# Kernel tuning notes

Hardware: AMD Instinct MI355X
Metric: run time of the kernel (lower is better)

The kernel has to match this reference:

```python
import jax, jax.numpy as jnp
import numpy as np

GAE_GAMMA = 0.99
GAE_LAMBDA = 0.95
T, N_ENVS = 4096, 2048


def setup_inputs() -> dict:
    key = jax.random.key(0)
    k1, k2, k3, k4 = jax.random.split(key, 4)
    rewards = jax.random.normal(k1, (T, N_ENVS), dtype=jnp.float32)
    values = jax.random.normal(k2, (T, N_ENVS), dtype=jnp.float32)
    next_values = jax.random.normal(k3, (T, N_ENVS), dtype=jnp.float32)
    next_dones = jax.random.randint(k4, (T, N_ENVS), 0, 2).astype(jnp.bool_)
    return {"rewards": rewards, "values": values,
            "next_values": next_values, "next_dones": next_dones}


def reference(rewards, values, next_values, next_dones):
    gamma = jnp.asarray(GAE_GAMMA, rewards.dtype)
    lam = jnp.asarray(GAE_LAMBDA, rewards.dtype)
    not_done = 1.0 - next_dones.astype(rewards.dtype)  # ~next_dones
    # deltas[t] = r[t] + gamma * V(s_{t+1}) * ~done[t] - V(s_t)
    deltas = rewards + gamma * next_values * not_done - values
    gae_discount = gamma * lam

    def step(running_gae, inp):
        delta_t, nd_t = inp
        g = delta_t + gae_discount * nd_t * running_gae
        return g, g

    init = jnp.zeros_like(rewards[0])
    # reverse-time scan over the recurrence
    _, adv = jax.lax.scan(step, init, (deltas, not_done), reverse=True)
    returns = adv + values
    return adv, returns
```

## Files before the change

kernel.cpp:

```cpp
#include <hip/hip_runtime.h>

#define TT    4096
#define NENV  2048
#define N4    (NENV / 4)
#define L     8
#define NCH   (TT / L)
#define NCGRP 2
#define NBLK  (NCH * NCGRP)
#define SUP   8
#define NSUP  (NCH / SUP)

#define GAMMA 0.99f
#define GL    (0.99f * 0.95f)

#define STEP_AB(r_, v_, nv_, dn_, A_, B_)                    \
    {                                                        \
        const float nd = (dn_) ? 0.0f : 1.0f;                \
        const float di = (r_) + GAMMA * (nv_) * nd - (v_);   \
        const float c  = GL * nd;                            \
        (B_) = di + c * (B_);                                \
        (A_) = c * (A_);                                     \
    }

#define STEP_OUT(r_, v_, nv_, dn_, g_, adv_, ret_)           \
    {                                                        \
        const float nd = (dn_) ? 0.0f : 1.0f;                \
        const float di = (r_) + GAMMA * (nv_) * nd - (v_);   \
        (g_) = di + GL * nd * (g_);                          \
        (adv_) = (g_);                                       \
        (ret_) = (g_) + (v_);                                \
    }

#define COMPOSE(Aj_, Bj_, A_, B_)                            \
    {                                                        \
        (B_) = (Bj_) + (Aj_) * (B_);                         \
        (A_) = (Aj_) * (A_);                                 \
    }

__global__ __launch_bounds__(256) void gae_k1(
    const float4* __restrict__ r4,  const float4* __restrict__ v4,
    const float4* __restrict__ nv4, const int4*   __restrict__ dn4,
    float4* __restrict__ wsA, float4* __restrict__ wsB)
{
    const int chunk = blockIdx.x / NCGRP;
    const int c4    = (blockIdx.x % NCGRP) * 256 + threadIdx.x;
    const int t0    = chunk * L;

    float Ax = 1.0f, Ay = 1.0f, Az = 1.0f, Aw = 1.0f;
    float Bx = 0.0f, By = 0.0f, Bz = 0.0f, Bw = 0.0f;
#pragma unroll
    for (int i = L - 1; i >= 0; --i) {
        const int idx = (t0 + i) * N4 + c4;
        const float4 r  = r4[idx];
        const float4 v  = v4[idx];
        const float4 nv = nv4[idx];
        const int4   dn = dn4[idx];
        STEP_AB(r.x, v.x, nv.x, dn.x, Ax, Bx);
        STEP_AB(r.y, v.y, nv.y, dn.y, Ay, By);
        STEP_AB(r.z, v.z, nv.z, dn.z, Az, Bz);
        STEP_AB(r.w, v.w, nv.w, dn.w, Aw, Bw);
    }
    wsA[chunk * N4 + c4] = make_float4(Ax, Ay, Az, Aw);
    wsB[chunk * N4 + c4] = make_float4(Bx, By, Bz, Bw);
}

__global__ __launch_bounds__(256) void gae_k2a(
    const float4* __restrict__ wsA, const float4* __restrict__ wsB,
    float4* __restrict__ supA, float4* __restrict__ supB)
{
    const int t  = blockIdx.x * 256 + threadIdx.x;
    const int s  = t >> 9;
    const int c4 = t & (N4 - 1);

    float Ax = 1.0f, Ay = 1.0f, Az = 1.0f, Aw = 1.0f;
    float Bx = 0.0f, By = 0.0f, Bz = 0.0f, Bw = 0.0f;
#pragma unroll
    for (int j = s * SUP + SUP - 1; j >= s * SUP; --j) {
        const float4 Aj = wsA[j * N4 + c4];
        const float4 Bj = wsB[j * N4 + c4];
        COMPOSE(Aj.x, Bj.x, Ax, Bx);
        COMPOSE(Aj.y, Bj.y, Ay, By);
        COMPOSE(Aj.z, Bj.z, Az, Bz);
        COMPOSE(Aj.w, Bj.w, Aw, Bw);
    }
    supA[s * N4 + c4] = make_float4(Ax, Ay, Az, Aw);
    supB[s * N4 + c4] = make_float4(Bx, By, Bz, Bw);
}

__global__ __launch_bounds__(64) void gae_k2b(
    const float* __restrict__ supA, const float* __restrict__ supB,
    float* __restrict__ gSup)
{
    const int col = blockIdx.x * 64 + threadIdx.x;
    float g = 0.0f;
#pragma unroll 8
    for (int s = NSUP - 1; s >= 0; --s) {
        gSup[s * NENV + col] = g;
        g = supB[s * NENV + col] + supA[s * NENV + col] * g;
    }
}

__global__ __launch_bounds__(256) void gae_k3(
    const float4* __restrict__ r4,  const float4* __restrict__ v4,
    const float4* __restrict__ nv4, const int4*   __restrict__ dn4,
    const float4* __restrict__ wsA, const float4* __restrict__ wsB,
    const float4* __restrict__ gSup4,
    float4* __restrict__ adv4, float4* __restrict__ ret4)
{
    const int chunk = blockIdx.x / NCGRP;
    const int c4    = (blockIdx.x % NCGRP) * 256 + threadIdx.x;
    const int s     = chunk / SUP;
    const int t0    = chunk * L;

    const float4 g0 = gSup4[s * N4 + c4];
    float gx = g0.x, gy = g0.y, gz = g0.z, gw = g0.w;
    for (int j = s * SUP + SUP - 1; j > chunk; --j) {
        const float4 Aj = wsA[j * N4 + c4];
        const float4 Bj = wsB[j * N4 + c4];
        gx = Bj.x + Aj.x * gx;
        gy = Bj.y + Aj.y * gy;
        gz = Bj.z + Aj.z * gz;
        gw = Bj.w + Aj.w * gw;
    }

#pragma unroll
    for (int i = L - 1; i >= 0; --i) {
        const int idx = (t0 + i) * N4 + c4;
        const float4 r  = r4[idx];
        const float4 v  = v4[idx];
        const float4 nv = nv4[idx];
        const int4   dn = dn4[idx];
        float4 a, t;
        STEP_OUT(r.x, v.x, nv.x, dn.x, gx, a.x, t.x);
        STEP_OUT(r.y, v.y, nv.y, dn.y, gy, a.y, t.y);
        STEP_OUT(r.z, v.z, nv.z, dn.z, gz, a.z, t.z);
        STEP_OUT(r.w, v.w, nv.w, dn.w, gw, a.w, t.w);
        adv4[idx] = a;
        ret4[idx] = t;
    }
}

extern "C" void kernel_launch(void* const* d_in, const int* in_sizes, int n_in,
                              void* d_out, int out_size, void* d_ws, size_t ws_size,
                              hipStream_t stream) {
    const float4* r4  = (const float4*)d_in[0];
    const float4* v4  = (const float4*)d_in[1];
    const float4* nv4 = (const float4*)d_in[2];
    const int4*   dn4 = (const int4*)d_in[3];

    float4* adv4 = (float4*)d_out;
    float4* ret4 = adv4 + (size_t)TT * N4;

    float4* wsA  = (float4*)d_ws;
    float4* wsB  = wsA  + (size_t)NCH * N4;
    float4* supA = wsB  + (size_t)NCH * N4;
    float4* supB = supA + (size_t)NSUP * N4;
    float4* gSup = supB + (size_t)NSUP * N4;

    gae_k1<<<NBLK, 256, 0, stream>>>(r4, v4, nv4, dn4, wsA, wsB);
    gae_k2a<<<(NSUP * N4) / 256, 256, 0, stream>>>(wsA, wsB, supA, supB);
    gae_k2b<<<NENV / 64, 64, 0, stream>>>((const float*)supA, (const float*)supB,
                                          (float*)gSup);
    gae_k3<<<NBLK, 256, 0, stream>>>(r4, v4, nv4, dn4, wsA, wsB,
                                     (const float4*)gSup, adv4, ret4);
}
```

Before: 202.9 us.

## Replace two-level chunk scan with single sequential carry scan and batched loads

The hierarchical middle stage (super-chunk compose plus serial scan plus per-chunk recomposition in the final kernel) is replaced by one kernel that serially walks all 512 chunk carries per column. It uses double-buffered register prefetch of 16 chunks and writes the incoming carry for each chunk in place over the B workspace. The first and last kernels now issue all eight timesteps' loads up front into registers, with an occupancy hint, to raise memory-level parallelism. This removes a launch and the redundant carry recomposition in the last kernel. In exchange, the serial middle kernel runs only 2048 threads over a 512-long dependent chain, which may be latency-bound.

New measurement: 210.1 us. 1.04x slower.

```diff
diff --git a/kernel.cpp b/kernel.cpp
--- a/kernel.cpp
+++ b/kernel.cpp
@@ -5,10 +5,7 @@
 #define N4    (NENV / 4)
 #define L     8
 #define NCH   (TT / L)
-#define NCGRP 2
-#define NBLK  (NCH * NCGRP)
-#define SUP   8
-#define NSUP  (NCH / SUP)
+#define NBLK  (NCH * 2)
 
 #define GAMMA 0.99f
 #define GL    (0.99f * 0.95f)
@@ -31,136 +28,119 @@
         (ret_) = (g_) + (v_);                                \
     }
 
-#define COMPOSE(Aj_, Bj_, A_, B_)                            \
-    {                                                        \
-        (B_) = (Bj_) + (Aj_) * (B_);                         \
-        (A_) = (Aj_) * (A_);                                 \
+#define P2_PREFETCH(abuf, bbuf, grp_)                        \
+    _Pragma("unroll")                                        \
+    for (int j = 0; j < 16; ++j) {                           \
+        const int c = NCH - 1 - (grp_) * 16 - j;             \
+        abuf[j] = As[c * NENV + col];                        \
+        bbuf[j] = Bs[c * NENV + col];                        \
     }
 
-__global__ __launch_bounds__(256) void gae_k1(
-    const float4* __restrict__ r4,  const float4* __restrict__ v4,
-    const float4* __restrict__ nv4, const int4*   __restrict__ dn4,
+#define P2_PROCESS(abuf, bbuf, grp_)                         \
+    _Pragma("unroll")                                        \
+    for (int j = 0; j < 16; ++j) {                           \
+        const int c = NCH - 1 - (grp_) * 16 - j;             \
+        Bs[c * NENV + col] = g;      \
+        g = fmaf(abuf[j], g, bbuf[j]);                       \
+    }
+
+__global__ __launch_bounds__(256, 4) void gae_k1(
+    const float4* __restrict__ rp,  const float4* __restrict__ vp,
+    const float4* __restrict__ np,  const int4*   __restrict__ dp,
     float4* __restrict__ wsA, float4* __restrict__ wsB)
 {
-    const int chunk = blockIdx.x / NCGRP;
-    const int c4    = (blockIdx.x % NCGRP) * 256 + threadIdx.x;
-    const int t0    = chunk * L;
+    const int chunk = (int)blockIdx.x >> 1;
+    const int c4    = (((int)blockIdx.x & 1) << 8) | (int)threadIdx.x;
+    const int base  = chunk * (L * N4) + c4;
 
-    float Ax = 1.0f, Ay = 1.0f, Az = 1.0f, Aw = 1.0f;
-    float Bx = 0.0f, By = 0.0f, Bz = 0.0f, Bw = 0.0f;
+    float4 R[L], V[L], NV[L]; int4 DN[L];
+#pragma unroll
+    for (int i = 0; i < L; ++i) R[i]  = rp[base + i * N4];
+#pragma unroll
+    for (int i = 0; i < L; ++i) NV[i] = np[base + i * N4];
+#pragma unroll
+    for (int i = 0; i < L; ++i) V[i]  = vp[base + i * N4];
+#pragma unroll
+    for (int i = 0; i < L; ++i) DN[i] = dp[base + i * N4];
+
+    float Ax = 1.f, Ay = 1.f, Az = 1.f, Aw = 1.f;
+    float Bx = 0.f, By = 0.f, Bz = 0.f, Bw = 0.f;
 #pragma unroll
     for (int i = L - 1; i >= 0; --i) {
-        const int idx = (t0 + i) * N4 + c4;
-        const float4 r  = r4[idx];
-        const float4 v  = v4[idx];
-        const float4 nv = nv4[idx];
-        const int4   dn = dn4[idx];
-        STEP_AB(r.x, v.x, nv.x, dn.x, Ax, Bx);
-        STEP_AB(r.y, v.y, nv.y, dn.y, Ay, By);
-        STEP_AB(r.z, v.z, nv.z, dn.z, Az, Bz);
-        STEP_AB(r.w, v.w, nv.w, dn.w, Aw, Bw);
+        STEP_AB(R[i].x, V[i].x, NV[i].x, DN[i].x, Ax, Bx);
+        STEP_AB(R[i].y, V[i].y, NV[i].y, DN[i].y, Ay, By);
+        STEP_AB(R[i].z, V[i].z, NV[i].z, DN[i].z, Az, Bz);
+        STEP_AB(R[i].w, V[i].w, NV[i].w, DN[i].w, Aw, Bw);
     }
     wsA[chunk * N4 + c4] = make_float4(Ax, Ay, Az, Aw);
     wsB[chunk * N4 + c4] = make_float4(Bx, By, Bz, Bw);
 }
 
-__global__ __launch_bounds__(256) void gae_k2a(
-    const float4* __restrict__ wsA, const float4* __restrict__ wsB,
-    float4* __restrict__ supA, float4* __restrict__ supB)
+__global__ __launch_bounds__(64) void gae_k2(
+    const float* __restrict__ As, float* __restrict__ Bs)
 {
-    const int t  = blockIdx.x * 256 + threadIdx.x;
-    const int s  = t >> 9;
-    const int c4 = t & (N4 - 1);
-
-    float Ax = 1.0f, Ay = 1.0f, Az = 1.0f, Aw = 1.0f;
-    float Bx = 0.0f, By = 0.0f, Bz = 0.0f, Bw = 0.0f;
-#pragma unroll
-    for (int j = s * SUP + SUP - 1; j >= s * SUP; --j) {
-        const float4 Aj = wsA[j * N4 + c4];
-        const float4 Bj = wsB[j * N4 + c4];
-        COMPOSE(Aj.x, Bj.x, Ax, Bx);
-        COMPOSE(Aj.y, Bj.y, Ay, By);
-        COMPOSE(Aj.z, Bj.z, Az, Bz);
-        COMPOSE(Aj.w, Bj.w, Aw, Bw);
-    }
-    supA[s * N4 + c4] = make_float4(Ax, Ay, Az, Aw);
-    supB[s * N4 + c4] = make_float4(Bx, By, Bz, Bw);
-}
-
-__global__ __launch_bounds__(64) void gae_k2b(
-    const float* __restrict__ supA, const float* __restrict__ supB,
-    float* __restrict__ gSup)
-{
-    const int col = blockIdx.x * 64 + threadIdx.x;
+    const int col = (int)blockIdx.x * 64 + (int)threadIdx.x;
+    float a0[16], b0[16], a1[16], b1[16];
     float g = 0.0f;
-#pragma unroll 8
-    for (int s = NSUP - 1; s >= 0; --s) {
-        gSup[s * NENV + col] = g;
-        g = supB[s * NENV + col] + supA[s * NENV + col] * g;
+    P2_PREFETCH(a0, b0, 0)
+    for (int grp = 0; grp < NCH / 16; grp += 2) {
+        P2_PREFETCH(a1, b1, grp + 1)
+        P2_PROCESS(a0, b0, grp)
+        if (grp + 2 < NCH / 16) { P2_PREFETCH(a0, b0, grp + 2) }
+        P2_PROCESS(a1, b1, grp + 1)
     }
 }
 
-__global__ __launch_bounds__(256) void gae_k3(
-    const float4* __restrict__ r4,  const float4* __restrict__ v4,
-    const float4* __restrict__ nv4, const int4*   __restrict__ dn4,
-    const float4* __restrict__ wsA, const float4* __restrict__ wsB,
-    const float4* __restrict__ gSup4,
+__global__ __launch_bounds__(256, 4) void gae_k3(
+    const float4* __restrict__ rp,  const float4* __restrict__ vp,
+    const float4* __restrict__ np,  const int4*   __restrict__ dp,
+    const float4* __restrict__ gin,
     float4* __restrict__ adv4, float4* __restrict__ ret4)
 {
-    const int chunk = blockIdx.x / NCGRP;
-    const int c4    = (blockIdx.x % NCGRP) * 256 + threadIdx.x;
-    const int s     = chunk / SUP;
-    const int t0    = chunk * L;
+    const int chunk = (int)blockIdx.x >> 1;
+    const int c4    = (((int)blockIdx.x & 1) << 8) | (int)threadIdx.x;
+    const int base  = chunk * (L * N4) + c4;
 
-    const float4 g0 = gSup4[s * N4 + c4];
+    const float4 g0 = gin[chunk * N4 + c4];
+
+    float4 R[L], V[L], NV[L]; int4 DN[L];
+#pragma unroll
+    for (int i = 0; i < L; ++i) R[i]  = rp[base + i * N4];
+#pragma unroll
+    for (int i = 0; i < L; ++i) NV[i] = np[base + i * N4];
+#pragma unroll
+    for (int i = 0; i < L; ++i) V[i]  = vp[base + i * N4];
+#pragma unroll
+    for (int i = 0; i < L; ++i) DN[i] = dp[base + i * N4];
+
     float gx = g0.x, gy = g0.y, gz = g0.z, gw = g0.w;
-    for (int j = s * SUP + SUP - 1; j > chunk; --j) {
-        const float4 Aj = wsA[j * N4 + c4];
-        const float4 Bj = wsB[j * N4 + c4];
-        gx = Bj.x + Aj.x * gx;
-        gy = Bj.y + Aj.y * gy;
-        gz = Bj.z + Aj.z * gz;
-        gw = Bj.w + Aj.w * gw;
-    }
-
 #pragma unroll
     for (int i = L - 1; i >= 0; --i) {
-        const int idx = (t0 + i) * N4 + c4;
-        const float4 r  = r4[idx];
-        const float4 v  = v4[idx];
-        const float4 nv = nv4[idx];
-        const int4   dn = dn4[idx];
         float4 a, t;
-        STEP_OUT(r.x, v.x, nv.x, dn.x, gx, a.x, t.x);
-        STEP_OUT(r.y, v.y, nv.y, dn.y, gy, a.y, t.y);
-        STEP_OUT(r.z, v.z, nv.z, dn.z, gz, a.z, t.z);
-        STEP_OUT(r.w, v.w, nv.w, dn.w, gw, a.w, t.w);
-        adv4[idx] = a;
-        ret4[idx] = t;
+        STEP_OUT(R[i].x, V[i].x, NV[i].x, DN[i].x, gx, a.x, t.x);
+        STEP_OUT(R[i].y, V[i].y, NV[i].y, DN[i].y, gy, a.y, t.y);
+        STEP_OUT(R[i].z, V[i].z, NV[i].z, DN[i].z, gz, a.z, t.z);
+        STEP_OUT(R[i].w, V[i].w, NV[i].w, DN[i].w, gw, a.w, t.w);
+        adv4[base + i * N4] = a;
+        ret4[base + i * N4] = t;
     }
 }
 
 extern "C" void kernel_launch(void* const* d_in, const int* in_sizes, int n_in,
                               void* d_out, int out_size, void* d_ws, size_t ws_size,
                               hipStream_t stream) {
-    const float4* r4  = (const float4*)d_in[0];
-    const float4* v4  = (const float4*)d_in[1];
-    const float4* nv4 = (const float4*)d_in[2];
-    const int4*   dn4 = (const int4*)d_in[3];
+    const float4* rp = (const float4*)d_in[0];
+    const float4* vp = (const float4*)d_in[1];
+    const float4* np = (const float4*)d_in[2];
+    const int4*   dp = (const int4*)d_in[3];
 
     float4* adv4 = (float4*)d_out;
     float4* ret4 = adv4 + (size_t)TT * N4;
 
-    float4* wsA  = (float4*)d_ws;
-    float4* wsB  = wsA  + (size_t)NCH * N4;
-    float4* supA = wsB  + (size_t)NCH * N4;
-    float4* supB = supA + (size_t)NSUP * N4;
-    float4* gSup = supB + (size_t)NSUP * N4;
+    float4* wsA = (float4*)d_ws;
+    float4* wsB = wsA + (size_t)NCH * N4;
 
-    gae_k1<<<NBLK, 256, 0, stream>>>(r4, v4, nv4, dn4, wsA, wsB);
-    gae_k2a<<<(NSUP * N4) / 256, 256, 0, stream>>>(wsA, wsB, supA, supB);
-    gae_k2b<<<NENV / 64, 64, 0, stream>>>((const float*)supA, (const float*)supB,
-                                          (float*)gSup);
-    gae_k3<<<NBLK, 256, 0, stream>>>(r4, v4, nv4, dn4, wsA, wsB,
-                                     (const float4*)gSup, adv4, ret4);
+    gae_k1<<<NBLK, 256, 0, stream>>>(rp, vp, np, dp, wsA, wsB);
+    gae_k2<<<NENV / 64, 64, 0, stream>>>((const float*)wsA, (float*)wsB);
+    gae_k3<<<NBLK, 256, 0, stream>>>(rp, vp, np, dp, wsB, adv4, ret4);
 }
```
